# Performance work log

Hardware: AMD Instinct MI355X
Metric: run time of the kernel (lower is better)

The kernel has to match this reference:

```python
import jax, jax.numpy as jnp
import numpy as np
import math

B, S, D_MODEL, H = 2, 2048, 1024, 16
HD = D_MODEL // H  # head_dim = 64


def _rope(x, seq_len):
    # x: [B, S, H, HD]; standard rotate-half RoPE with base 10000
    d = x.shape[-1]
    inv_freq = 1.0 / (10000.0 ** (jnp.arange(0, d, 2, dtype=jnp.float32) / d))
    t = jnp.arange(seq_len, dtype=jnp.float32)
    freqs = t[:, None] * inv_freq[None, :]              # [S, HD/2]
    emb = jnp.concatenate([freqs, freqs], axis=-1)      # [S, HD]
    cos = jnp.cos(emb)[None, :, None, :]
    sin = jnp.sin(emb)[None, :, None, :]
    x1, x2 = jnp.split(x, 2, axis=-1)
    rot = jnp.concatenate([-x2, x1], axis=-1)
    return x * cos + rot * sin


def setup_inputs() -> dict:
    key = jax.random.key(0)
    ks = jax.random.split(key, 11)
    s = 1.0 / math.sqrt(D_MODEL)
    return {
        "query": jax.random.normal(ks[0], (B, S, D_MODEL), jnp.float32),
        "keys": jax.random.normal(ks[1], (B, S, D_MODEL), jnp.float32),
        "values": jax.random.normal(ks[2], (B, S, D_MODEL), jnp.float32),
        "Wq": jax.random.normal(ks[3], (D_MODEL, D_MODEL), jnp.float32) * s,
        "bq": jnp.zeros((D_MODEL,), jnp.float32),
        "Wk": jax.random.normal(ks[4], (D_MODEL, D_MODEL), jnp.float32) * s,
        "bk": jnp.zeros((D_MODEL,), jnp.float32),
        "Wv": jax.random.normal(ks[5], (D_MODEL, D_MODEL), jnp.float32) * s,
        "bv": jnp.zeros((D_MODEL,), jnp.float32),
        "Wo": jax.random.normal(ks[6], (D_MODEL, D_MODEL), jnp.float32) * s,
        "bo": jnp.zeros((D_MODEL,), jnp.float32),
    }


def reference(query, keys, values, Wq, bq, Wk, bk, Wv, bv, Wo, bo):
    b, s, _ = query.shape
    scale = math.sqrt(HD)
    q = (query @ Wq.T + bq).reshape(b, s, H, HD)   # [B,S,H,HD]
    k = (keys @ Wk.T + bk).reshape(b, s, H, HD)
    v = (values @ Wv.T + bv).reshape(b, s, H, HD)
    q = _rope(q, s)
    k = _rope(k, s)
    # scores: [B,H,Sq,Sk]
    scores = jnp.einsum('bqhd,bkhd->bhqk', q, k)
    causal = jnp.tril(jnp.ones((s, s), dtype=bool))[None, None]
    scores = jnp.where(causal, scores, -jnp.inf) / scale
    attn = jax.nn.softmax(scores, axis=-1)
    ctx = jnp.einsum('bhqk,bkhd->bqhd', attn, v).reshape(b, s, H * HD)
    out = ctx @ Wo.T + bo
    return out, attn
```

## Files before the change

kernel.cpp:

```cpp
#include <hip/hip_runtime.h>
#include <hip/hip_bf16.h>
#include <stdint.h>
#include <math.h>


typedef __attribute__((ext_vector_type(8))) __bf16 bf16x8;
typedef __attribute__((ext_vector_type(4))) float f32x4;

__device__ __forceinline__ unsigned short f2bf(float f) {
  unsigned int u = __float_as_uint(f);
  u += 0x7fffu + ((u >> 16) & 1u);
  return (unsigned short)(u >> 16);
}

typedef const __attribute__((address_space(1))) unsigned int* gas_ptr;
typedef __attribute__((address_space(3))) unsigned int* las_ptr;
__device__ __forceinline__ void glds16(const void* g, void* l) {
  __builtin_amdgcn_global_load_lds((gas_ptr)g, (las_ptr)l, 16, 0, 0);
}

__global__ __launch_bounds__(256) void rope_table(float2* __restrict__ tab) {
  const int i = blockIdx.x * 256 + threadIdx.x;
  const int spos = i >> 5, d = i & 31;
  const double invf = pow(10000.0, -(double)d / 32.0);
  const double ang = (double)spos * invf;
  double sn, cs;
  sincos(ang, &sn, &cs);
  tab[i] = make_float2((float)cs, (float)sn);
}

__global__ __launch_bounds__(256) void cvt_all(
    const float* __restrict__ a0, const float* __restrict__ a1,
    const float* __restrict__ a2, const float* __restrict__ w0,
    const float* __restrict__ w1, const float* __restrict__ w2,
    const float* __restrict__ w3, unsigned short* __restrict__ ws) {
  const int z = blockIdx.z;
  const float* src;
  unsigned short* dst;
  int n;
  if (z == 0)      { src = a0; dst = ws;             n = 4194304; }
  else if (z == 1) { src = a1; dst = ws + 4194304;   n = 4194304; }
  else if (z == 2) { src = a2; dst = ws + 8388608;   n = 4194304; }
  else if (z == 3) { src = w0; dst = ws + 12582912;  n = 1048576; }
  else if (z == 4) { src = w1; dst = ws + 13631488;  n = 1048576; }
  else if (z == 5) { src = w2; dst = ws + 14680064;  n = 1048576; }
  else             { src = w3; dst = ws + 15728640;  n = 1048576; }
  const int n4 = n >> 2;
  for (int i = blockIdx.x * 256 + threadIdx.x; i < n4; i += gridDim.x * 256) {
    float4 f = ((const float4*)src)[i];
    ushort4 u;
    u.x = f2bf(f.x); u.y = f2bf(f.y); u.z = f2bf(f.z); u.w = f2bf(f.w);
    ((ushort4*)dst)[i] = u;
  }
}

__global__ __launch_bounds__(256) void gemm_qkv(
    const unsigned short* __restrict__ xq, const unsigned short* __restrict__ xk,
    const unsigned short* __restrict__ xv, const unsigned short* __restrict__ wq,
    const unsigned short* __restrict__ wk, const unsigned short* __restrict__ wv,
    const float* __restrict__ bq, const float* __restrict__ bk,
    const float* __restrict__ bv, const float2* __restrict__ rtab,
    unsigned short* __restrict__ qo, unsigned short* __restrict__ ko,
    unsigned short* __restrict__ vo) {
  const int z = blockIdx.z;
  const unsigned short* A = (z == 0) ? xq : (z == 1) ? xk : xv;
  const unsigned short* W = (z == 0) ? wq : (z == 1) ? wk : wv;
  const float* bias = (z == 0) ? bq : (z == 1) ? bk : bv;
  unsigned short* out = (z == 0) ? qo : (z == 1) ? ko : vo;

  const int t = threadIdx.x;
  const int lane = t & 63, wave = t >> 6;
  const int wr = wave >> 1, wc = wave & 1;
  const int lrow = lane & 15, lkb = lane >> 4;
  const int m0 = blockIdx.y * 128, n0 = blockIdx.x * 128;

  __shared__ __align__(16) unsigned short abuf[4096];
  __shared__ __align__(16) unsigned short bbuf[4096];

  f32x4 acc[4][4] = {};

  for (int k0 = 0; k0 < 1024; k0 += 32) {
    __syncthreads();
#pragma unroll
    for (int i = 0; i < 2; ++i) {
      int slot = i * 256 + t;
      int kb = slot >> 7, row = slot & 127;
      glds16(A + (size_t)(m0 + row) * 1024 + k0 + kb * 8, &abuf[slot * 8]);
      glds16(W + (size_t)(n0 + row) * 1024 + k0 + kb * 8, &bbuf[slot * 8]);
    }
    __syncthreads();
    bf16x8 af[4], bfr[4];
#pragma unroll
    for (int mi = 0; mi < 4; ++mi)
      af[mi] = *(const bf16x8*)&abuf[(lkb * 128 + wr * 64 + mi * 16 + lrow) * 8];
#pragma unroll
    for (int ni = 0; ni < 4; ++ni)
      bfr[ni] = *(const bf16x8*)&bbuf[(lkb * 128 + wc * 64 + ni * 16 + lrow) * 8];
#pragma unroll
    for (int mi = 0; mi < 4; ++mi)
#pragma unroll
      for (int ni = 0; ni < 4; ++ni)
        acc[mi][ni] = __builtin_amdgcn_mfma_f32_16x16x32_bf16(af[mi], bfr[ni],
                                                              acc[mi][ni], 0, 0, 0);
  }

  const int nbase = n0 + wc * 64;
  float bias_v[4];
#pragma unroll
  for (int ni = 0; ni < 4; ++ni) bias_v[ni] = bias[nbase + ni * 16 + lrow];

  const int mbase = m0 + wr * 64 + 4 * lkb;
  const bool rope = (z < 2);
  const float qsc = (z == 0) ? 0.125f : 1.0f;

#pragma unroll
  for (int mi = 0; mi < 4; ++mi) {
#pragma unroll
    for (int r = 0; r < 4; ++r) {
      const int m = mbase + mi * 16 + r;
      const int bidx = m >> 11, spos = m & 2047;
      float vals[4];
#pragma unroll
      for (int ni = 0; ni < 4; ++ni) vals[ni] = acc[mi][ni][r] + bias_v[ni];
      if (rope) {
#pragma unroll
        for (int ni = 0; ni < 2; ++ni) {
          const int d = ni * 16 + lrow;
          const float2 cs2 = rtab[spos * 32 + d];
          float x1 = vals[ni], x2 = vals[ni + 2];
          vals[ni] = (x1 * cs2.x - x2 * cs2.y) * qsc;
          vals[ni + 2] = (x2 * cs2.x + x1 * cs2.y) * qsc;
        }
      }
#pragma unroll
      for (int ni = 0; ni < 4; ++ni) {
        const int n = nbase + ni * 16 + lrow;
        const int h = n >> 6, d = n & 63;
        out[(size_t)((bidx * 16 + h) * 2048 + spos) * 64 + d] = f2bf(vals[ni]);
      }
    }
  }
}

__global__ __launch_bounds__(256) void gemm_out(
    const unsigned short* __restrict__ A, const unsigned short* __restrict__ W,
    const float* __restrict__ bias, float* __restrict__ out) {
  const int t = threadIdx.x;
  const int lane = t & 63, wave = t >> 6;
  const int wr = wave >> 1, wc = wave & 1;
  const int lrow = lane & 15, lkb = lane >> 4;
  const int m0 = blockIdx.y * 128, n0 = blockIdx.x * 128;

  __shared__ __align__(16) unsigned short abuf[4096];
  __shared__ __align__(16) unsigned short bbuf[4096];

  f32x4 acc[4][4] = {};

  for (int k0 = 0; k0 < 1024; k0 += 32) {
    __syncthreads();
#pragma unroll
    for (int i = 0; i < 2; ++i) {
      int slot = i * 256 + t;
      int kb = slot >> 7, row = slot & 127;
      glds16(A + (size_t)(m0 + row) * 1024 + k0 + kb * 8, &abuf[slot * 8]);
      glds16(W + (size_t)(n0 + row) * 1024 + k0 + kb * 8, &bbuf[slot * 8]);
    }
    __syncthreads();
    bf16x8 af[4], bfr[4];
#pragma unroll
    for (int mi = 0; mi < 4; ++mi)
      af[mi] = *(const bf16x8*)&abuf[(lkb * 128 + wr * 64 + mi * 16 + lrow) * 8];
#pragma unroll
    for (int ni = 0; ni < 4; ++ni)
      bfr[ni] = *(const bf16x8*)&bbuf[(lkb * 128 + wc * 64 + ni * 16 + lrow) * 8];
#pragma unroll
    for (int mi = 0; mi < 4; ++mi)
#pragma unroll
      for (int ni = 0; ni < 4; ++ni)
        acc[mi][ni] = __builtin_amdgcn_mfma_f32_16x16x32_bf16(af[mi], bfr[ni],
                                                              acc[mi][ni], 0, 0, 0);
  }

  const int nbase = n0 + wc * 64;
  float bias_v[4];
#pragma unroll
  for (int ni = 0; ni < 4; ++ni) bias_v[ni] = bias[nbase + ni * 16 + lrow];
  const int mbase = m0 + wr * 64 + 4 * lkb;
#pragma unroll
  for (int mi = 0; mi < 4; ++mi)
#pragma unroll
    for (int r = 0; r < 4; ++r) {
      const int m = mbase + mi * 16 + r;
      float* orow = out + (size_t)m * 1024 + nbase;
#pragma unroll
      for (int ni = 0; ni < 4; ++ni)
        orow[ni * 16 + lrow] = acc[mi][ni][r] + bias_v[ni];
    }
}

__global__ __launch_bounds__(256) void transpose_v(
    const unsigned short* __restrict__ v, unsigned short* __restrict__ vt) {
  const int s0 = blockIdx.x * 64;
  const int bh = blockIdx.y;
  __shared__ __align__(16) unsigned short tile[64][80];
  const int t = threadIdx.x;
  {
    const int row = t >> 2, cb = t & 3;
    const unsigned short* src = v + (size_t)(bh * 2048 + s0 + row) * 64 + cb * 16;
    *(uint4*)&tile[row][cb * 16] = *(const uint4*)src;
    *(uint4*)&tile[row][cb * 16 + 8] = *(const uint4*)(src + 8);
  }
  __syncthreads();
  {
    const int d = t >> 2, sc = t & 3;
    __align__(16) unsigned short tmp[16];
#pragma unroll
    for (int u = 0; u < 16; ++u) tmp[u] = tile[sc * 16 + u][d];
    unsigned short* dst = vt + (size_t)(bh * 64 + d) * 2048 + s0 + sc * 16;
    *(uint4*)dst = *(const uint4*)&tmp[0];
    *(uint4*)(dst + 8) = *(const uint4*)&tmp[8];
  }
}

__global__ __launch_bounds__(256) void attn_kernel(
    const unsigned short* __restrict__ Q, const unsigned short* __restrict__ Km,
    const unsigned short* __restrict__ Vt, float* __restrict__ attn,
    unsigned short* __restrict__ ctx) {
  const int qt = blockIdx.x;
  const int bh = blockIdx.y;
  const int t = threadIdx.x;
  const int lane = t & 63, wave = t >> 6;
  const int lrow = lane & 15, lg = lane >> 4;
  const int q0 = qt * 64;
  const int wq0 = q0 + wave * 16;

  const unsigned short* Qb = Q + (size_t)bh * 2048 * 64;
  const unsigned short* Kb = Km + (size_t)bh * 2048 * 64;
  const unsigned short* Vb = Vt + (size_t)bh * 64 * 2048;
  float* attn_b = attn + (size_t)bh * 2048 * 2048;

  __shared__ __align__(16) unsigned short kbuf[4096];
  __shared__ __align__(16) unsigned short vbuf[4096];
  __shared__ __align__(16) unsigned short pbuf[4][1024];

  bf16x8 qf[2];
#pragma unroll
  for (int dk = 0; dk < 2; ++dk)
    qf[dk] = *(const bf16x8*)(Qb + (size_t)(wq0 + lrow) * 64 + dk * 32 + lg * 8);

  const int nkt = qt + 1;
  float m_loc[4] = {-1e30f, -1e30f, -1e30f, -1e30f};
  float l_loc[4] = {0.f, 0.f, 0.f, 0.f};

  for (int kt = 0; kt < nkt; ++kt) {
    const int k0 = kt * 64;
    __syncthreads();
#pragma unroll
    for (int i = 0; i < 2; ++i) {
      int slot = i * 256 + t;
      int kb = slot >> 6, row = slot & 63;
      glds16(Kb + (size_t)(k0 + row) * 64 + kb * 8, &kbuf[slot * 8]);
    }
    __syncthreads();
    f32x4 s[4] = {};
#pragma unroll
    for (int fc = 0; fc < 4; ++fc)
#pragma unroll
      for (int dk = 0; dk < 2; ++dk) {
        bf16x8 kf = *(const bf16x8*)&kbuf[((dk * 4 + lg) * 64 + fc * 16 + lrow) * 8];
        s[fc] = __builtin_amdgcn_mfma_f32_16x16x32_bf16(qf[dk], kf, s[fc], 0, 0, 0);
      }
#pragma unroll
    for (int r = 0; r < 4; ++r) {
      const int qg = wq0 + 4 * lg + r;
      float nm = m_loc[r];
      float vv[4];
      bool ok[4];
#pragma unroll
      for (int fc = 0; fc < 4; ++fc) {
        const int kg = k0 + fc * 16 + lrow;
        ok[fc] = (kg <= qg);
        vv[fc] = ok[fc] ? s[fc][r] : -1e30f;
        nm = fmaxf(nm, vv[fc]);
      }
      const float scale_old = __expf(m_loc[r] - nm);
      float sum = 0.f;
#pragma unroll
      for (int fc = 0; fc < 4; ++fc) sum += ok[fc] ? __expf(vv[fc] - nm) : 0.f;
      l_loc[r] = l_loc[r] * scale_old + sum;
      m_loc[r] = nm;
    }
  }

  float m_row[4], linv[4];
#pragma unroll
  for (int r = 0; r < 4; ++r) {
    float m = m_loc[r], l = l_loc[r];
#pragma unroll
    for (int off = 1; off < 16; off <<= 1) {
      float mo = __shfl_xor(m, off);
      float lo = __shfl_xor(l, off);
      float nm = fmaxf(m, mo);
      l = l * __expf(m - nm) + lo * __expf(mo - nm);
      m = nm;
    }
    m_row[r] = m;
    linv[r] = 1.0f / l;
  }

  f32x4 oa[4] = {};
  for (int kt = 0; kt < nkt; ++kt) {
    const int k0 = kt * 64;
    __syncthreads();
#pragma unroll
    for (int i = 0; i < 2; ++i) {
      int slot = i * 256 + t;
      int kb = slot >> 6, row = slot & 63;
      glds16(Kb + (size_t)(k0 + row) * 64 + kb * 8, &kbuf[slot * 8]);
      glds16(Vb + (size_t)row * 2048 + k0 + kb * 8, &vbuf[slot * 8]);
    }
    __syncthreads();
    f32x4 s[4] = {};
#pragma unroll
    for (int fc = 0; fc < 4; ++fc)
#pragma unroll
      for (int dk = 0; dk < 2; ++dk) {
        bf16x8 kf = *(const bf16x8*)&kbuf[((dk * 4 + lg) * 64 + fc * 16 + lrow) * 8];
        s[fc] = __builtin_amdgcn_mfma_f32_16x16x32_bf16(qf[dk], kf, s[fc], 0, 0, 0);
      }
#pragma unroll
    for (int r = 0; r < 4; ++r) {
      const int qg = wq0 + 4 * lg + r;
      const int q_ = 4 * lg + r;
      float* arow = attn_b + (size_t)qg * 2048 + k0;
#pragma unroll
      for (int fc = 0; fc < 4; ++fc) {
        const int kg = k0 + fc * 16 + lrow;
        const float p = (kg <= qg) ? __expf(s[fc][r] - m_row[r]) * linv[r] : 0.f;
        arow[fc * 16 + lrow] = p;
        const int k_ = fc * 16 + lrow;
        const int dl = q_ + 16 * ((k_ >> 3) & 3);
        const int kk = k_ >> 5, j = k_ & 7;
        int byteo = (kk * 64 + dl) * 16 + j * 2;
        byteo ^= ((kk * 8 + (dl >> 3)) & 7) << 4;
        *(unsigned short*)((char*)pbuf[wave] + byteo) = f2bf(p);
      }
    }
#pragma unroll
    for (int kk = 0; kk < 2; ++kk) {
      int rbyte = (kk * 64 + lane) * 16;
      rbyte ^= ((kk * 8 + (lane >> 3)) & 7) << 4;
      bf16x8 pa = *(const bf16x8*)((char*)pbuf[wave] + rbyte);
#pragma unroll
      for (int fd = 0; fd < 4; ++fd) {
        bf16x8 vf = *(const bf16x8*)&vbuf[((kk * 4 + lg) * 64 + fd * 16 + lrow) * 8];
        oa[fd] = __builtin_amdgcn_mfma_f32_16x16x32_bf16(pa, vf, oa[fd], 0, 0, 0);
      }
    }
  }

  const int zc0 = nkt * 16;
  for (int rr = 0; rr < 16; ++rr) {
    const int qg = wq0 + rr;
    float4* arow = (float4*)(attn_b + (size_t)qg * 2048);
    for (int c = zc0 + lane; c < 512; c += 64)
      arow[c] = make_float4(0.f, 0.f, 0.f, 0.f);
  }

  const int bidx = bh >> 4, h = bh & 15;
#pragma unroll
  for (int fd = 0; fd < 4; ++fd)
#pragma unroll
    for (int r = 0; r < 4; ++r) {
      const int qg = wq0 + 4 * lg + r;
      ctx[(size_t)(bidx * 2048 + qg) * 1024 + h * 64 + fd * 16 + lrow] =
          f2bf(oa[fd][r]);
    }
}

extern "C" void kernel_launch(void* const* d_in, const int* in_sizes, int n_in,
                              void* d_out, int out_size, void* d_ws, size_t ws_size,
                              hipStream_t stream) {
  const float* q_in = (const float*)d_in[0];
  const float* k_in = (const float*)d_in[1];
  const float* v_in = (const float*)d_in[2];
  const float* Wq = (const float*)d_in[3];
  const float* bq = (const float*)d_in[4];
  const float* Wk = (const float*)d_in[5];
  const float* bk = (const float*)d_in[6];
  const float* Wv = (const float*)d_in[7];
  const float* bv = (const float*)d_in[8];
  const float* Wo = (const float*)d_in[9];
  const float* bo = (const float*)d_in[10];

  unsigned short* ws = (unsigned short*)d_ws;
  float* outp = (float*)d_out;

  const size_t OXQ = 0, OXK = 4194304, OXV = 8388608;
  const size_t OWQ = 12582912, OWK = 13631488, OWV = 14680064, OWO = 15728640;
  const size_t OQ = 16777216, OK = 20971520, OV = 25165824;
  const size_t OTAB = 29360128;
  const size_t OVT = OXK;
  const size_t OCTX = OXQ;
  float2* rtab = (float2*)(ws + OTAB);

  rope_table<<<dim3(256), 256, 0, stream>>>(rtab);
  cvt_all<<<dim3(512, 1, 7), 256, 0, stream>>>(q_in, k_in, v_in, Wq, Wk, Wv, Wo, ws);
  gemm_qkv<<<dim3(8, 32, 3), 256, 0, stream>>>(ws + OXQ, ws + OXK, ws + OXV,
                                               ws + OWQ, ws + OWK, ws + OWV,
                                               bq, bk, bv, rtab,
                                               ws + OQ, ws + OK, ws + OV);
  transpose_v<<<dim3(32, 32), 256, 0, stream>>>(ws + OV, ws + OVT);
  attn_kernel<<<dim3(32, 32), 256, 0, stream>>>(ws + OQ, ws + OK, ws + OVT,
                                                outp + 4194304, ws + OCTX);
  gemm_out<<<dim3(8, 32), 256, 0, stream>>>(ws + OCTX, ws + OWO, bo, outp);
}
```

Baseline: 355.2 us.

## Coalesce attn-prob stores via LDS staging, double K-tile in GEMMs and stats pass

```diff
diff --git a/kernel.cpp b/kernel.cpp
--- a/kernel.cpp
+++ b/kernel.cpp
@@ -74,34 +74,37 @@
   const int lrow = lane & 15, lkb = lane >> 4;
   const int m0 = blockIdx.y * 128, n0 = blockIdx.x * 128;
 
-  __shared__ __align__(16) unsigned short abuf[4096];
-  __shared__ __align__(16) unsigned short bbuf[4096];
+  __shared__ __align__(16) unsigned short abuf[8192];
+  __shared__ __align__(16) unsigned short bbuf[8192];
 
   f32x4 acc[4][4] = {};
 
-  for (int k0 = 0; k0 < 1024; k0 += 32) {
-    __syncthreads();
-#pragma unroll
-    for (int i = 0; i < 2; ++i) {
+  for (int k0 = 0; k0 < 1024; k0 += 64) {
+    __syncthreads();
+#pragma unroll
+    for (int i = 0; i < 4; ++i) {
       int slot = i * 256 + t;
       int kb = slot >> 7, row = slot & 127;
       glds16(A + (size_t)(m0 + row) * 1024 + k0 + kb * 8, &abuf[slot * 8]);
       glds16(W + (size_t)(n0 + row) * 1024 + k0 + kb * 8, &bbuf[slot * 8]);
     }
     __syncthreads();
-    bf16x8 af[4], bfr[4];
-#pragma unroll
-    for (int mi = 0; mi < 4; ++mi)
-      af[mi] = *(const bf16x8*)&abuf[(lkb * 128 + wr * 64 + mi * 16 + lrow) * 8];
-#pragma unroll
-    for (int ni = 0; ni < 4; ++ni)
-      bfr[ni] = *(const bf16x8*)&bbuf[(lkb * 128 + wc * 64 + ni * 16 + lrow) * 8];
-#pragma unroll
-    for (int mi = 0; mi < 4; ++mi)
+#pragma unroll
+    for (int ks = 0; ks < 2; ++ks) {
+      bf16x8 af[4], bfr[4];
+#pragma unroll
+      for (int mi = 0; mi < 4; ++mi)
+        af[mi] = *(const bf16x8*)&abuf[((ks * 4 + lkb) * 128 + wr * 64 + mi * 16 + lrow) * 8];
 #pragma unroll
       for (int ni = 0; ni < 4; ++ni)
-        acc[mi][ni] = __builtin_amdgcn_mfma_f32_16x16x32_bf16(af[mi], bfr[ni],
-                                                              acc[mi][ni], 0, 0, 0);
+        bfr[ni] = *(const bf16x8*)&bbuf[((ks * 4 + lkb) * 128 + wc * 64 + ni * 16 + lrow) * 8];
+#pragma unroll
+      for (int mi = 0; mi < 4; ++mi)
+#pragma unroll
+        for (int ni = 0; ni < 4; ++ni)
+          acc[mi][ni] = __builtin_amdgcn_mfma_f32_16x16x32_bf16(af[mi], bfr[ni],
+                                                                acc[mi][ni], 0, 0, 0);
+    }
   }
 
   const int nbase = n0 + wc * 64;
@@ -151,34 +154,37 @@
   const int lrow = lane & 15, lkb = lane >> 4;
   const int m0 = blockIdx.y * 128, n0 = blockIdx.x * 128;
 
-  __shared__ __align__(16) unsigned short abuf[4096];
-  __shared__ __align__(16) unsigned short bbuf[4096];
+  __shared__ __align__(16) unsigned short abuf[8192];
+  __shared__ __align__(16) unsigned short bbuf[8192];
 
   f32x4 acc[4][4] = {};
 
-  for (int k0 = 0; k0 < 1024; k0 += 32) {
-    __syncthreads();
-#pragma unroll
-    for (int i = 0; i < 2; ++i) {
+  for (int k0 = 0; k0 < 1024; k0 += 64) {
+    __syncthreads();
+#pragma unroll
+    for (int i = 0; i < 4; ++i) {
       int slot = i * 256 + t;
       int kb = slot >> 7, row = slot & 127;
       glds16(A + (size_t)(m0 + row) * 1024 + k0 + kb * 8, &abuf[slot * 8]);
       glds16(W + (size_t)(n0 + row) * 1024 + k0 + kb * 8, &bbuf[slot * 8]);
     }
     __syncthreads();
-    bf16x8 af[4], bfr[4];
-#pragma unroll
-    for (int mi = 0; mi < 4; ++mi)
-      af[mi] = *(const bf16x8*)&abuf[(lkb * 128 + wr * 64 + mi * 16 + lrow) * 8];
-#pragma unroll
-    for (int ni = 0; ni < 4; ++ni)
-      bfr[ni] = *(const bf16x8*)&bbuf[(lkb * 128 + wc * 64 + ni * 16 + lrow) * 8];
-#pragma unroll
-    for (int mi = 0; mi < 4; ++mi)
+#pragma unroll
+    for (int ks = 0; ks < 2; ++ks) {
+      bf16x8 af[4], bfr[4];
+#pragma unroll
+      for (int mi = 0; mi < 4; ++mi)
+        af[mi] = *(const bf16x8*)&abuf[((ks * 4 + lkb) * 128 + wr * 64 + mi * 16 + lrow) * 8];
 #pragma unroll
       for (int ni = 0; ni < 4; ++ni)
-        acc[mi][ni] = __builtin_amdgcn_mfma_f32_16x16x32_bf16(af[mi], bfr[ni],
-                                                              acc[mi][ni], 0, 0, 0);
+        bfr[ni] = *(const bf16x8*)&bbuf[((ks * 4 + lkb) * 128 + wc * 64 + ni * 16 + lrow) * 8];
+#pragma unroll
+      for (int mi = 0; mi < 4; ++mi)
+#pragma unroll
+        for (int ni = 0; ni < 4; ++ni)
+          acc[mi][ni] = __builtin_amdgcn_mfma_f32_16x16x32_bf16(af[mi], bfr[ni],
+                                                                acc[mi][ni], 0, 0, 0);
+    }
   }
 
   const int nbase = n0 + wc * 64;
@@ -241,7 +247,7 @@
 
   __shared__ __align__(16) unsigned short kbuf[4096];
   __shared__ __align__(16) unsigned short vbuf[4096];
-  __shared__ __align__(16) unsigned short pbuf[4][1024];
+  __shared__ __align__(16) float pfbuf[4 * 16 * 66];
 
   bf16x8 qf[2];
 #pragma unroll
@@ -252,22 +258,13 @@
   float m_loc[4] = {-1e30f, -1e30f, -1e30f, -1e30f};
   float l_loc[4] = {0.f, 0.f, 0.f, 0.f};
 
-  for (int kt = 0; kt < nkt; ++kt) {
-    const int k0 = kt * 64;
-    __syncthreads();
-#pragma unroll
-    for (int i = 0; i < 2; ++i) {
-      int slot = i * 256 + t;
-      int kb = slot >> 6, row = slot & 63;
-      glds16(Kb + (size_t)(k0 + row) * 64 + kb * 8, &kbuf[slot * 8]);
-    }
-    __syncthreads();
+  auto mlupdate = [&](const unsigned short* buf, int kbase) {
     f32x4 s[4] = {};
 #pragma unroll
     for (int fc = 0; fc < 4; ++fc)
 #pragma unroll
       for (int dk = 0; dk < 2; ++dk) {
-        bf16x8 kf = *(const bf16x8*)&kbuf[((dk * 4 + lg) * 64 + fc * 16 + lrow) * 8];
+        bf16x8 kf = *(const bf16x8*)&buf[((dk * 4 + lg) * 64 + fc * 16 + lrow) * 8];
         s[fc] = __builtin_amdgcn_mfma_f32_16x16x32_bf16(qf[dk], kf, s[fc], 0, 0, 0);
       }
 #pragma unroll
@@ -278,7 +275,7 @@
       bool ok[4];
 #pragma unroll
       for (int fc = 0; fc < 4; ++fc) {
-        const int kg = k0 + fc * 16 + lrow;
+        const int kg = kbase + fc * 16 + lrow;
         ok[fc] = (kg <= qg);
         vv[fc] = ok[fc] ? s[fc][r] : -1e30f;
         nm = fmaxf(nm, vv[fc]);
@@ -290,6 +287,23 @@
       l_loc[r] = l_loc[r] * scale_old + sum;
       m_loc[r] = nm;
     }
+  };
+
+  for (int kt = 0; kt < nkt; kt += 2) {
+    const int k0 = kt * 64;
+    const bool two = (kt + 1) < nkt;
+    __syncthreads();
+#pragma unroll
+    for (int i = 0; i < 2; ++i) {
+      int slot = i * 256 + t;
+      int cb = slot >> 6, row = slot & 63;
+      glds16(Kb + (size_t)(k0 + row) * 64 + cb * 8, &kbuf[slot * 8]);
+      if (two)
+        glds16(Kb + (size_t)(k0 + 64 + row) * 64 + cb * 8, &vbuf[slot * 8]);
+    }
+    __syncthreads();
+    mlupdate(kbuf, k0);
+    if (two) mlupdate(vbuf, k0 + 64);
   }
 
   float m_row[4], linv[4];
@@ -309,15 +323,16 @@
   }
 
   f32x4 oa[4] = {};
+  float* pf = pfbuf + wave * (16 * 66);
   for (int kt = 0; kt < nkt; ++kt) {
     const int k0 = kt * 64;
     __syncthreads();
 #pragma unroll
     for (int i = 0; i < 2; ++i) {
       int slot = i * 256 + t;
-      int kb = slot >> 6, row = slot & 63;
-      glds16(Kb + (size_t)(k0 + row) * 64 + kb * 8, &kbuf[slot * 8]);
-      glds16(Vb + (size_t)row * 2048 + k0 + kb * 8, &vbuf[slot * 8]);
+      int cb = slot >> 6, row = slot & 63;
+      glds16(Kb + (size_t)(k0 + row) * 64 + cb * 8, &kbuf[slot * 8]);
+      glds16(Vb + (size_t)row * 2048 + k0 + cb * 8, &vbuf[slot * 8]);
     }
     __syncthreads();
     f32x4 s[4] = {};
@@ -331,30 +346,37 @@
 #pragma unroll
     for (int r = 0; r < 4; ++r) {
       const int qg = wq0 + 4 * lg + r;
-      const int q_ = 4 * lg + r;
-      float* arow = attn_b + (size_t)qg * 2048 + k0;
 #pragma unroll
       for (int fc = 0; fc < 4; ++fc) {
         const int kg = k0 + fc * 16 + lrow;
         const float p = (kg <= qg) ? __expf(s[fc][r] - m_row[r]) * linv[r] : 0.f;
-        arow[fc * 16 + lrow] = p;
-        const int k_ = fc * 16 + lrow;
-        const int dl = q_ + 16 * ((k_ >> 3) & 3);
-        const int kk = k_ >> 5, j = k_ & 7;
-        int byteo = (kk * 64 + dl) * 16 + j * 2;
-        byteo ^= ((kk * 8 + (dl >> 3)) & 7) << 4;
-        *(unsigned short*)((char*)pbuf[wave] + byteo) = f2bf(p);
+        pf[(4 * lg + r) * 66 + fc * 16 + lrow] = p;
       }
     }
 #pragma unroll
     for (int kk = 0; kk < 2; ++kk) {
-      int rbyte = (kk * 64 + lane) * 16;
-      rbyte ^= ((kk * 8 + (lane >> 3)) & 7) << 4;
-      bf16x8 pa = *(const bf16x8*)((char*)pbuf[wave] + rbyte);
+      const float* pr = pf + (lane & 15) * 66 + kk * 32 + (lane >> 4) * 8;
+      float2 f0 = *(const float2*)(pr + 0);
+      float2 f1 = *(const float2*)(pr + 2);
+      float2 f2v = *(const float2*)(pr + 4);
+      float2 f3 = *(const float2*)(pr + 6);
+      bf16x8 pa = {(__bf16)f0.x, (__bf16)f0.y, (__bf16)f1.x, (__bf16)f1.y,
+                   (__bf16)f2v.x, (__bf16)f2v.y, (__bf16)f3.x, (__bf16)f3.y};
 #pragma unroll
       for (int fd = 0; fd < 4; ++fd) {
         bf16x8 vf = *(const bf16x8*)&vbuf[((kk * 4 + lg) * 64 + fd * 16 + lrow) * 8];
         oa[fd] = __builtin_amdgcn_mfma_f32_16x16x32_bf16(pa, vf, oa[fd], 0, 0, 0);
+      }
+    }
+    {
+      const int rl = lane >> 2, ch = lane & 3;
+      const float* srow = pf + rl * 66 + ch * 16;
+      float4* dst = (float4*)(attn_b + (size_t)(wq0 + rl) * 2048 + k0 + ch * 16);
+#pragma unroll
+      for (int i2 = 0; i2 < 4; ++i2) {
+        float2 a = *(const float2*)(srow + i2 * 4);
+        float2 b2 = *(const float2*)(srow + i2 * 4 + 2);
+        dst[i2] = make_float4(a.x, a.y, b2.x, b2.y);
       }
     }
   }
```

Result: slower. 394.3 us (+11.0%).
